# Kernel tuning notes

Hardware: AMD Instinct MI355X
Metric: run time of the kernel (lower is better)

The kernel has to match this reference:

```python
import jax, jax.numpy as jnp
import numpy as np

N = 100000      # nodes
E = 1600000     # edges (avg degree 16)
IN_C = 128
OUT_C = 64
HID = 2 * OUT_C  # 128


def setup_inputs() -> dict:
    key = jax.random.key(0)
    ks = jax.random.split(key, 8)
    x = jax.random.normal(ks[0], (N, IN_C), dtype=jnp.float32)
    edge_index = jax.random.randint(ks[1], (2, E), 0, N, dtype=jnp.int32)
    # Glorot-ish init for GCN weight matrices, zero bias (PyG default)
    w1 = jax.random.normal(ks[2], (IN_C, HID), dtype=jnp.float32) / np.sqrt(IN_C)
    b1 = jnp.zeros((HID,), jnp.float32)
    w_mu = jax.random.normal(ks[3], (HID, OUT_C), dtype=jnp.float32) / np.sqrt(HID)
    b_mu = jnp.zeros((OUT_C,), jnp.float32)
    w_ls = jax.random.normal(ks[4], (HID, OUT_C), dtype=jnp.float32) / np.sqrt(HID)
    b_ls = jnp.zeros((OUT_C,), jnp.float32)
    return {"x": x, "edge_index": edge_index, "w1": w1, "b1": b1,
            "w_mu": w_mu, "b_mu": b_mu, "w_ls": w_ls, "b_ls": b_ls}


def _gcn_conv(h, w, b, src, dst, norm, n):
    # linear transform, then normalized sparse aggregation src -> dst
    h = h @ w                                   # [N, out]
    msg = h[src] * norm[:, None]                # [E+N, out] gather
    out = jax.ops.segment_sum(msg, dst, num_segments=n)  # scatter-add
    return out + b


def reference(x, edge_index, w1, b1, w_mu, b_mu, w_ls, b_ls):
    n = x.shape[0]
    # GCN normalization with self-loops (edge_weight=None -> all ones)
    loops = jnp.arange(n, dtype=edge_index.dtype)
    src = jnp.concatenate([edge_index[0], loops])
    dst = jnp.concatenate([edge_index[1], loops])
    ew = jnp.ones(src.shape[0], dtype=x.dtype)
    deg = jax.ops.segment_sum(ew, dst, num_segments=n)
    dinv = jnp.where(deg > 0, jax.lax.rsqrt(jnp.maximum(deg, 1e-12)), 0.0)
    norm = dinv[src] * ew * dinv[dst]           # D^-1/2 A_hat D^-1/2

    h = jax.nn.relu(_gcn_conv(x, w1, b1, src, dst, norm, n))
    mu = _gcn_conv(h, w_mu, b_mu, src, dst, norm, n)
    logstd = _gcn_conv(h, w_ls, b_ls, src, dst, norm, n)
    return (mu, logstd)
```

## Files before the change

### kernel.cpp

```cpp
#include <hip/hip_runtime.h>
#include <hip/hip_bf16.h>

#define CH 128
#define OC 64
#define NBINS 1024
#define NCHK  256
#define BSH   7

typedef __attribute__((ext_vector_type(4))) float f32x4;
typedef __attribute__((ext_vector_type(8))) float f32x8;
typedef __attribute__((ext_vector_type(8))) short bf16x8;
typedef __attribute__((ext_vector_type(8))) ushort u16x8;

static __device__ __forceinline__ float bf2f(ushort u) {
  return __uint_as_float(((unsigned)u) << 16);
}
static __device__ __forceinline__ ushort f2bf(float f) {
  __hip_bfloat16 h = __float2bfloat16(f);
  return *reinterpret_cast<ushort*>(&h);
}
static __device__ __forceinline__ void fma8(float w, u16x8 v, f32x8& a) {
#pragma unroll
  for (int j = 0; j < 8; j++) a[j] = fmaf(w, bf2f((ushort)v[j]), a[j]);
}

__global__ void k_pre(const float* __restrict__ x, ushort* __restrict__ y, int nx,
                      const float* __restrict__ w1, const float* __restrict__ wmu,
                      const float* __restrict__ wls, const float* __restrict__ bmu,
                      const float* __restrict__ bls, ushort* __restrict__ Wt0,
                      ushort* __restrict__ Wt1, float* __restrict__ bc) {
  int gid = blockIdx.x * 256 + threadIdx.x;
  int i = gid * 4;
  if (i < nx) {
    float4 v = *(const float4*)&x[i];
    ushort4 o; o.x = f2bf(v.x); o.y = f2bf(v.y); o.z = f2bf(v.z); o.w = f2bf(v.w);
    *(ushort4*)&y[i] = o;
  }
  if (gid < 16384) {
    int c = gid >> 7, k = gid & 127;
    Wt0[c * 128 + k] = f2bf(w1[k * 128 + c]);
    float v = (c < 64) ? wmu[k * 64 + c] : wls[k * 64 + (c - 64)];
    Wt1[c * 128 + k] = f2bf(v);
    if (gid < 128) bc[gid] = (gid < 64) ? bmu[gid] : bls[gid - 64];
  }
}


__global__ __launch_bounds__(256) void k_s1(const int* __restrict__ dst,
                                            int* __restrict__ bcntT, int ne, int cs) {
  __shared__ int h[NBINS];
  for (int j = threadIdx.x; j < NBINS; j += 256) h[j] = 0;
  __syncthreads();
  int e0 = blockIdx.x * cs, e1 = min(e0 + cs, ne);
  for (int e = e0 + threadIdx.x; e < e1; e += 256)
    atomicAdd(&h[dst[e] >> BSH], 1);
  __syncthreads();
  for (int j = threadIdx.x; j < NBINS; j += 256)
    bcntT[j * NCHK + blockIdx.x] = h[j];
}

__global__ __launch_bounds__(256) void k_s2a(const int* __restrict__ bcntT,
                                             int* __restrict__ curT,
                                             int* __restrict__ total) {
  __shared__ int s[NCHK];
  int b = blockIdx.x, t = threadIdx.x;
  int v = bcntT[b * NCHK + t];
  s[t] = v; __syncthreads();
  for (int off = 1; off < NCHK; off <<= 1) {
    int u = (t >= off) ? s[t - off] : 0;
    __syncthreads();
    s[t] += u;
    __syncthreads();
  }
  curT[b * NCHK + t] = s[t] - v;
  if (t == NCHK - 1) total[b] = s[t];
}

__global__ void k_s2b(const int* __restrict__ total, int* __restrict__ base) {
  __shared__ int s[256];
  int t = threadIdx.x;
  int loc[4]; int sum = 0;
#pragma unroll
  for (int j = 0; j < 4; j++) { loc[j] = total[t * 4 + j]; sum += loc[j]; }
  s[t] = sum; __syncthreads();
  int own = sum;
  for (int off = 1; off < 256; off <<= 1) {
    int u = (t >= off) ? s[t - off] : 0;
    __syncthreads();
    s[t] += u;
    __syncthreads();
  }
  int excl = s[t] - own;
#pragma unroll
  for (int j = 0; j < 4; j++) { base[t * 4 + j] = excl; excl += loc[j]; }
  if (t == 255) base[NBINS] = excl;
}

__global__ __launch_bounds__(256) void k_s3(const int* __restrict__ src,
    const int* __restrict__ dst, const int* __restrict__ curT,
    const int* __restrict__ base, unsigned* __restrict__ rec, int ne, int cs) {
  __shared__ int lcur[NBINS];
  int blk = blockIdx.x;
  for (int b = threadIdx.x; b < NBINS; b += 256)
    lcur[b] = curT[b * NCHK + blk] + base[b];
  __syncthreads();
  int e0 = blk * cs, e1 = min(e0 + cs, ne);
  for (int e = e0 + threadIdx.x; e < e1; e += 256) {
    int d = dst[e], sv = src[e];
    int pos = atomicAdd(&lcur[d >> BSH], 1);
    rec[pos] = ((unsigned)sv << BSH) | (unsigned)(d & 127);
  }
}

__global__ __launch_bounds__(256) void k_s4a(const unsigned* __restrict__ rec,
    const int* __restrict__ base, int* __restrict__ deg, int* __restrict__ rowptr,
    float* __restrict__ dinv, int nn) {
  __shared__ int h[128];
  __shared__ int sc[128];
  int b = blockIdx.x, tid = threadIdx.x;
  if (tid < 128) h[tid] = 0;
  __syncthreads();
  int r0 = base[b], r1 = base[b + 1];
  for (int r = r0 + tid; r < r1; r += 256)
    atomicAdd(&h[rec[r] & 127], 1);
  __syncthreads();
  if (tid < 128) sc[tid] = h[tid];
  __syncthreads();
  for (int off = 1; off < 128; off <<= 1) {
    int v = 0;
    if (tid < 128 && tid >= off) v = sc[tid - off];
    __syncthreads();
    if (tid < 128) sc[tid] += v;
    __syncthreads();
  }
  if (tid < 128) {
    int node = (b << BSH) + tid;
    if (node < nn) {
      int d = h[tid];
      deg[node] = d;
      rowptr[node] = r0 + sc[tid] - d;
      dinv[node] = rsqrtf((float)(d + 1));
    }
  }
}

__global__ __launch_bounds__(256) void k_s5(const unsigned* __restrict__ rec,
    const int* __restrict__ base, const int* __restrict__ rowptr,
    const int* __restrict__ deg, unsigned* __restrict__ csr, int nn) {
  __shared__ int lcur[128];
  int b = blockIdx.x, tid = threadIdx.x;
  if (tid < 128) {
    int node = (b << BSH) + tid;
    lcur[tid] = (node < nn) ? rowptr[node] : 0;
  }
  __syncthreads();
  int r0 = base[b], r1 = base[b + 1];
  for (int r = r0 + tid; r < r1; r += 256) {
    unsigned rc = rec[r];
    int s = (int)(rc >> BSH);
    int pos = atomicAdd(&lcur[rc & 127], 1);
    unsigned ds = (unsigned)min(deg[s], 32767);
    csr[pos] = (unsigned)s | (ds << 17);
  }
}

static __device__ __forceinline__ f32x8 gather_core(const ushort* __restrict__ in,
    const int* __restrict__ rowptr, const int* __restrict__ deg,
    const unsigned* __restrict__ csr, const float* __restrict__ dinv,
    int i, int lane16, float& di_out) {
  size_t loff = (size_t)lane16 * 8;
  int beg = rowptr[i];
  int cnt = deg[i];
  float di = dinv[i];
  u16x8 xv = *(const u16x8*)&in[(size_t)i * CH + loff];
  f32x8 acc = {0.f, 0.f, 0.f, 0.f, 0.f, 0.f, 0.f, 0.f};

  unsigned rec[8]; u16x8 row[4];
#pragma unroll
  for (int j = 0; j < 8; j++) rec[j] = (j < cnt) ? csr[beg + j] : 0u;
#pragma unroll
  for (int j = 0; j < 4; j++)
    if (j < cnt) row[j] = *(const u16x8*)&in[(size_t)(rec[j] & 0x1FFFFu) * CH + loff];

  int k = 0;
  while (cnt - k > 4) {
    unsigned nrec[4]; u16x8 nrow[4];
#pragma unroll
    for (int j = 0; j < 4; j++)
      nrec[j] = (k + 8 + j < cnt) ? csr[beg + k + 8 + j] : 0u;
#pragma unroll
    for (int j = 0; j < 4; j++)
      nrow[j] = (k + 4 + j < cnt)
              ? *(const u16x8*)&in[(size_t)(rec[4 + j] & 0x1FFFFu) * CH + loff]
              : row[j];
#pragma unroll
    for (int j = 0; j < 4; j++) {
      float w = rsqrtf((float)((rec[j] >> 17) + 1u));
      fma8(w, row[j], acc);
    }
#pragma unroll
    for (int j = 0; j < 4; j++) { rec[j] = rec[4 + j]; rec[4 + j] = nrec[j]; row[j] = nrow[j]; }
    k += 4;
  }
#pragma unroll
  for (int j = 0; j < 4; j++) {
    if (k + j < cnt) {
      float w = rsqrtf((float)((rec[j] >> 17) + 1u));
      fma8(w, row[j], acc);
    }
  }
  fma8(di, xv, acc);
  di_out = di;
  return acc;
}

__global__ __launch_bounds__(256) void k_agg0(const ushort* __restrict__ in,
                      ushort* __restrict__ o16,
                      const int* __restrict__ rowptr, const int* __restrict__ deg,
                      const unsigned* __restrict__ csr, const float* __restrict__ dinv,
                      int n) {
  int i = blockIdx.x * 16 + (threadIdx.x >> 4);
  if (i >= n) return;
  int lane = threadIdx.x & 15;
  float di;
  f32x8 acc = gather_core(in, rowptr, deg, csr, dinv, i, lane, di);
  u16x8 o;
#pragma unroll
  for (int j = 0; j < 8; j++) o[j] = (short)f2bf(acc[j] * di);
  *(u16x8*)&o16[(size_t)i * CH + lane * 8] = o;
}

__global__ __launch_bounds__(256) void k_fused(const ushort* __restrict__ A,
    const ushort* __restrict__ Wt0, const float* __restrict__ b1,
    const ushort* __restrict__ Wt1, ushort* __restrict__ P, int ntiles) {
  __shared__ ushort hs[16][136];
  int colg = threadIdx.x >> 6;
  int lane = threadIdx.x & 63;
  int l15 = lane & 15;
  int lk = (lane >> 4) * 8;
  bf16x8 bfrag1[2][4], bfrag2[2][4];
  float bias1[2];
#pragma unroll
  for (int ct = 0; ct < 2; ct++) {
    int bcol = colg * 32 + ct * 16 + l15;
#pragma unroll
    for (int kt = 0; kt < 4; kt++) {
      bfrag1[ct][kt] = *(const bf16x8*)&Wt0[(size_t)bcol * 128 + kt * 32 + lk];
      bfrag2[ct][kt] = *(const bf16x8*)&Wt1[(size_t)bcol * 128 + kt * 32 + lk];
    }
    bias1[ct] = b1[bcol];
  }
  for (int t = blockIdx.x; t < ntiles; t += gridDim.x) {
    const ushort* ap = &A[(size_t)(t * 16 + l15) * CH + lk];
    bf16x8 af[4];
#pragma unroll
    for (int kt = 0; kt < 4; kt++) af[kt] = *(const bf16x8*)&ap[kt * 32];
    f32x4 a1[2] = {{0.f, 0.f, 0.f, 0.f}, {0.f, 0.f, 0.f, 0.f}};
#pragma unroll
    for (int ct = 0; ct < 2; ct++)
#pragma unroll
      for (int kt = 0; kt < 4; kt++)
        a1[ct] = __builtin_amdgcn_mfma_f32_16x16x32_bf16(af[kt], bfrag1[ct][kt], a1[ct], 0, 0, 0);
#pragma unroll
    for (int ct = 0; ct < 2; ct++) {
      int col = colg * 32 + ct * 16 + l15;
#pragma unroll
      for (int r = 0; r < 4; r++)
        hs[(lane >> 4) * 4 + r][col] = f2bf(fmaxf(a1[ct][r] + bias1[ct], 0.f));
    }
    __syncthreads();
    bf16x8 af2[4];
#pragma unroll
    for (int kt = 0; kt < 4; kt++) af2[kt] = *(const bf16x8*)&hs[l15][kt * 32 + lk];
    f32x4 a2[2] = {{0.f, 0.f, 0.f, 0.f}, {0.f, 0.f, 0.f, 0.f}};
#pragma unroll
    for (int ct = 0; ct < 2; ct++)
#pragma unroll
      for (int kt = 0; kt < 4; kt++)
        a2[ct] = __builtin_amdgcn_mfma_f32_16x16x32_bf16(af2[kt], bfrag2[ct][kt], a2[ct], 0, 0, 0);
#pragma unroll
    for (int ct = 0; ct < 2; ct++) {
      int col = colg * 32 + ct * 16 + l15;
#pragma unroll
      for (int r = 0; r < 4; r++) {
        int node = t * 16 + (lane >> 4) * 4 + r;
        P[(size_t)node * CH + col] = f2bf(a2[ct][r]);
      }
    }
    __syncthreads();
  }
}

__global__ __launch_bounds__(256) void k_aggout(const ushort* __restrict__ in,
                      float* __restrict__ oA, float* __restrict__ oB,
                      const float* __restrict__ bc,
                      const int* __restrict__ rowptr, const int* __restrict__ deg,
                      const unsigned* __restrict__ csr, const float* __restrict__ dinv,
                      int n) {
  int i = blockIdx.x * 16 + (threadIdx.x >> 4);
  if (i >= n) return;
  int lane = threadIdx.x & 15;
  float di;
  f32x8 acc = gather_core(in, rowptr, deg, csr, dinv, i, lane, di);
  f32x8 b8 = *(const f32x8*)&bc[lane * 8];
  f32x8 o;
#pragma unroll
  for (int j = 0; j < 8; j++) o[j] = acc[j] * di + b8[j];
  if (lane < 8) *(f32x8*)&oA[(size_t)i * OC + lane * 8] = o;
  else          *(f32x8*)&oB[(size_t)i * OC + (lane - 8) * 8] = o;
}


extern "C" void kernel_launch(void* const* d_in, const int* in_sizes, int n_in,
                              void* d_out, int out_size, void* d_ws, size_t ws_size,
                              hipStream_t stream) {
  const float* x   = (const float*)d_in[0];
  const int*   ei  = (const int*)d_in[1];
  const float* w1  = (const float*)d_in[2];
  const float* b1  = (const float*)d_in[3];
  const float* wmu = (const float*)d_in[4];
  const float* bmu = (const float*)d_in[5];
  const float* wls = (const float*)d_in[6];
  const float* bls = (const float*)d_in[7];
  float* out = (float*)d_out;

  const int nn = in_sizes[0] / CH;
  const int ne = in_sizes[1] / 2;
  const int* srcp = ei;
  const int* dstp = ei + ne;

  ushort*   B0   = (ushort*)d_ws;
  ushort*   B1   = B0 + (size_t)nn * CH;
  unsigned* csr  = (unsigned*)(B1 + (size_t)nn * CH);
  int*      deg  = (int*)(csr + ne);
  int*      rowptr = deg + nn;
  float*    dinv = (float*)(rowptr + nn);
  ushort*   Wt0  = (ushort*)(dinv + nn);
  ushort*   Wt1  = Wt0 + 128 * 128;
  float*    bc   = (float*)(Wt1 + 128 * 128);

  unsigned* rec  = (unsigned*)B1;
  int*      bcntT= (int*)(rec + ne);
  int*      curT = bcntT + NBINS * NCHK;
  int*      btot = curT + NBINS * NCHK;
  int*      bbase= btot + NBINS;

  const int NBUK = (nn + 127) >> BSH;
  const int cs = (ne + NCHK - 1) / NCHK;

  k_s1 <<<NCHK, 256, 0, stream>>>(dstp, bcntT, ne, cs);
  k_s2a<<<NBINS, NCHK, 0, stream>>>(bcntT, curT, btot);
  k_s2b<<<1, 256, 0, stream>>>(btot, bbase);
  k_s3 <<<NCHK, 256, 0, stream>>>(srcp, dstp, curT, bbase, rec, ne, cs);
  k_s4a<<<NBUK, 256, 0, stream>>>(rec, bbase, deg, rowptr, dinv, nn);
  k_s5 <<<NBUK, 256, 0, stream>>>(rec, bbase, rowptr, deg, csr, nn);
  k_pre<<<((nn * CH / 4) + 255) / 256, 256, 0, stream>>>(x, B0, nn * CH,
                                 w1, wmu, wls, bmu, bls, Wt0, Wt1, bc);

  const int AB = (nn + 15) / 16;
  const int ntiles = nn / 16;

  k_agg0<<<AB, 256, 0, stream>>>(B0, B1, rowptr, deg, csr, dinv, nn);
  k_fused<<<1024, 256, 0, stream>>>(B1, Wt0, b1, Wt1, B0, ntiles);
  k_aggout<<<AB, 256, 0, stream>>>(B0, out, out + (size_t)nn * OC, bc,
                                   rowptr, deg, csr, dinv, nn);
}
```

Baseline: 215.7 us.

## Deepen gather prefetch and double-buffer fused MLP tile loop

The neighbor gather in both aggregation kernels now keeps eight rows and twelve CSR records in flight instead of four and eight, to hide more gather latency per node. The fused two-layer MFMA kernel prefetches the next tile's A fragments during the current tile's compute. It also double-buffers its shared-memory staging so the trailing barrier can be removed, and the grid doubles to 2048 blocks. The trade-off is higher register pressure, which may reduce occupancy in the gather kernels.

Result: slower. 230.3 us (+6.8%).

```diff
diff --git a/kernel.cpp b/kernel.cpp
--- a/kernel.cpp
+++ b/kernel.cpp
@@ -175,35 +175,37 @@
   u16x8 xv = *(const u16x8*)&in[(size_t)i * CH + loff];
   f32x8 acc = {0.f, 0.f, 0.f, 0.f, 0.f, 0.f, 0.f, 0.f};
 
-  unsigned rec[8]; u16x8 row[4];
-#pragma unroll
-  for (int j = 0; j < 8; j++) rec[j] = (j < cnt) ? csr[beg + j] : 0u;
-#pragma unroll
-  for (int j = 0; j < 4; j++)
+  unsigned rec[12]; u16x8 row[8];
+#pragma unroll
+  for (int j = 0; j < 12; j++) rec[j] = (j < cnt) ? csr[beg + j] : 0u;
+#pragma unroll
+  for (int j = 0; j < 8; j++)
     if (j < cnt) row[j] = *(const u16x8*)&in[(size_t)(rec[j] & 0x1FFFFu) * CH + loff];
 
   int k = 0;
-  while (cnt - k > 4) {
+  while (cnt - k > 8) {
     unsigned nrec[4]; u16x8 nrow[4];
 #pragma unroll
     for (int j = 0; j < 4; j++)
-      nrec[j] = (k + 8 + j < cnt) ? csr[beg + k + 8 + j] : 0u;
+      nrec[j] = (k + 12 + j < cnt) ? csr[beg + k + 12 + j] : 0u;
 #pragma unroll
     for (int j = 0; j < 4; j++)
-      nrow[j] = (k + 4 + j < cnt)
-              ? *(const u16x8*)&in[(size_t)(rec[4 + j] & 0x1FFFFu) * CH + loff]
-              : row[j];
+      nrow[j] = (k + 8 + j < cnt)
+              ? *(const u16x8*)&in[(size_t)(rec[8 + j] & 0x1FFFFu) * CH + loff]
+              : row[4 + j];
 #pragma unroll
     for (int j = 0; j < 4; j++) {
       float w = rsqrtf((float)((rec[j] >> 17) + 1u));
       fma8(w, row[j], acc);
     }
 #pragma unroll
-    for (int j = 0; j < 4; j++) { rec[j] = rec[4 + j]; rec[4 + j] = nrec[j]; row[j] = nrow[j]; }
+    for (int j = 0; j < 8; j++) rec[j] = rec[j + 4];
+#pragma unroll
+    for (int j = 0; j < 4; j++) { rec[8 + j] = nrec[j]; row[j] = row[4 + j]; row[4 + j] = nrow[j]; }
     k += 4;
   }
 #pragma unroll
-  for (int j = 0; j < 4; j++) {
+  for (int j = 0; j < 8; j++) {
     if (k + j < cnt) {
       float w = rsqrtf((float)((rec[j] >> 17) + 1u));
       fma8(w, row[j], acc);
@@ -233,7 +235,7 @@
 __global__ __launch_bounds__(256) void k_fused(const ushort* __restrict__ A,
     const ushort* __restrict__ Wt0, const float* __restrict__ b1,
     const ushort* __restrict__ Wt1, ushort* __restrict__ P, int ntiles) {
-  __shared__ ushort hs[16][136];
+  __shared__ ushort hs[2][16][136];
   int colg = threadIdx.x >> 6;
   int lane = threadIdx.x & 63;
   int l15 = lane & 15;
@@ -250,11 +252,23 @@
     }
     bias1[ct] = b1[bcol];
   }
-  for (int t = blockIdx.x; t < ntiles; t += gridDim.x) {
+  int G = gridDim.x;
+  int t = blockIdx.x;
+  int buf = 0;
+  bf16x8 af[4];
+  if (t < ntiles) {
     const ushort* ap = &A[(size_t)(t * 16 + l15) * CH + lk];
-    bf16x8 af[4];
 #pragma unroll
     for (int kt = 0; kt < 4; kt++) af[kt] = *(const bf16x8*)&ap[kt * 32];
+  }
+  for (; t < ntiles; t += G) {
+    int tn = t + G;
+    bf16x8 afn[4];
+    if (tn < ntiles) {
+      const ushort* apn = &A[(size_t)(tn * 16 + l15) * CH + lk];
+#pragma unroll
+      for (int kt = 0; kt < 4; kt++) afn[kt] = *(const bf16x8*)&apn[kt * 32];
+    }
     f32x4 a1[2] = {{0.f, 0.f, 0.f, 0.f}, {0.f, 0.f, 0.f, 0.f}};
 #pragma unroll
     for (int ct = 0; ct < 2; ct++)
@@ -266,12 +280,12 @@
       int col = colg * 32 + ct * 16 + l15;
 #pragma unroll
       for (int r = 0; r < 4; r++)
-        hs[(lane >> 4) * 4 + r][col] = f2bf(fmaxf(a1[ct][r] + bias1[ct], 0.f));
+        hs[buf][(lane >> 4) * 4 + r][col] = f2bf(fmaxf(a1[ct][r] + bias1[ct], 0.f));
     }
     __syncthreads();
     bf16x8 af2[4];
 #pragma unroll
-    for (int kt = 0; kt < 4; kt++) af2[kt] = *(const bf16x8*)&hs[l15][kt * 32 + lk];
+    for (int kt = 0; kt < 4; kt++) af2[kt] = *(const bf16x8*)&hs[buf][l15][kt * 32 + lk];
     f32x4 a2[2] = {{0.f, 0.f, 0.f, 0.f}, {0.f, 0.f, 0.f, 0.f}};
 #pragma unroll
     for (int ct = 0; ct < 2; ct++)
@@ -287,7 +301,9 @@
         P[(size_t)node * CH + col] = f2bf(a2[ct][r]);
       }
     }
-    __syncthreads();
+    buf ^= 1;
+#pragma unroll
+    for (int kt = 0; kt < 4; kt++) af[kt] = afn[kt];
   }
 }
 
@@ -361,7 +377,7 @@
   const int ntiles = nn / 16;
 
   k_agg0<<<AB, 256, 0, stream>>>(B0, B1, rowptr, deg, csr, dinv, nn);
-  k_fused<<<1024, 256, 0, stream>>>(B1, Wt0, b1, Wt1, B0, ntiles);
+  k_fused<<<2048, 256, 0, stream>>>(B1, Wt0, b1, Wt1, B0, ntiles);
   k_aggout<<<AB, 256, 0, stream>>>(B0, out, out + (size_t)nn * OC, bc,
                                    rowptr, deg, csr, dinv, nn);
 }
```
